# Kernel optimization log

Hardware: AMD Instinct MI355X
Metric: run time of the kernel (lower is better)

## Reference

```python
import jax, jax.numpy as jnp
import numpy as np


def setup_inputs() -> dict:
    key = jax.random.key(0)
    ks = jax.random.split(key, 6)
    B, S, H, I, E, V = 8, 512, 512, 2048, 16, 32000
    std = 0.02
    return {
        "hidden_states": jax.random.normal(ks[0], (B, S, H), dtype=jnp.float32),
        "expert_probs": jax.random.uniform(ks[1], (B, E), dtype=jnp.float32),
        "Wg": jax.random.normal(ks[2], (E, I, H), dtype=jnp.float32) * std,
        "Wu": jax.random.normal(ks[3], (E, I, H), dtype=jnp.float32) * std,
        "Wd": jax.random.normal(ks[4], (E, H, I), dtype=jnp.float32) * (std * 0.5),
        "Wout": jax.random.normal(ks[5], (V, H), dtype=jnp.float32) * std,
        "top_k": 2,
    }


def reference(hidden_states, expert_probs, Wg, Wu, Wd, Wout, top_k):
    # Per-sample top-k routing (routing is over the batch dim, not tokens).
    topk_probs, topk_ids = jax.lax.top_k(expert_probs, top_k)  # (B, k)
    topk_probs = topk_probs / (jnp.sum(topk_probs, axis=-1, keepdims=True) + 1e-8)

    B, S, H = hidden_states.shape
    combined = jnp.zeros((B, S, H), dtype=hidden_states.dtype)
    for k in range(top_k):  # top_k is a small static int (2)
        eid = topk_ids[:, k]                     # (B,)
        wg = Wg[eid]                             # (B, I, H) gathered expert weights
        wu = Wu[eid]                             # (B, I, H)
        wd = Wd[eid]                             # (B, H, I)
        gate = jax.nn.silu(jnp.einsum('bsh,bih->bsi', hidden_states, wg))
        up = jnp.einsum('bsh,bih->bsi', hidden_states, wu)
        out = jnp.einsum('bsi,bhi->bsh', gate * up, wd)
        combined = combined + topk_probs[:, k][:, None, None] * out

    # Shared output projection -> logits (B, S, V)
    return jnp.einsum('bsh,vh->bsv', combined, Wout)
```

## Files before the change

kernel.cpp:

```cpp
#include <hip/hip_runtime.h>
#include <hip/hip_bf16.h>
#include <cstdint>

typedef __attribute__((ext_vector_type(8))) short bf16x8;
typedef __attribute__((ext_vector_type(4))) float f32x4;

#define MFMA16(a, b, c) __builtin_amdgcn_mfma_f32_16x16x32_bf16((a), (b), (c), 0, 0, 0)

__device__ __forceinline__ ushort f2bf(float x) {
  union { float f; uint32_t u; } c; c.f = x;
  uint32_t r = (c.u + 0x7FFFu + ((c.u >> 16) & 1u)) >> 16;
  return (ushort)r;
}

__device__ __forceinline__ void gload_lds16(const ushort* g, ushort* l) {
  __builtin_amdgcn_global_load_lds((__attribute__((address_space(1))) void*)g,
                                   (__attribute__((address_space(3))) void*)l, 16, 0, 0);
}

template <int NW, int INSTR>
__device__ __forceinline__ void stageT(const ushort* __restrict__ tileBase, int ld,
                                       ushort* lds, int wid, int lane) {
#pragma unroll
  for (int q = 0; q < INSTR; q++) {
    int r = (wid * INSTR + q) * 8 + (lane >> 3);
    int cb = ((lane & 7) * 16) ^ ((r & 7) << 4);
    gload_lds16(tileBase + (long)r * ld + (cb >> 1), lds + (wid * INSTR + q) * 512);
  }
}

__device__ __forceinline__ bf16x8 frag_read(const ushort* lds, int r, int kb) {
  int off = r * 128 + (kb ^ ((r & 7) << 4));
  return *(const bf16x8*)((const char*)lds + off);
}

template <int INSTR>
__device__ __forceinline__ void stage32(const ushort* __restrict__ tileBase, int ld,
                                        ushort* lds, int wid, int lane) {
#pragma unroll
  for (int q = 0; q < INSTR; q++) {
    int r = (wid * INSTR + q) * 16 + (lane >> 2);
    int cb = ((lane & 3) ^ ((r >> 1) & 3)) * 16;
    gload_lds16(tileBase + (long)r * ld + (cb >> 1), lds + (wid * INSTR + q) * 512);
  }
}

__device__ __forceinline__ bf16x8 frag_read32(const ushort* lds, int r, int kslot) {
  int off = r * 64 + ((kslot ^ ((r >> 1) & 3)) * 16);
  return *(const bf16x8*)((const char*)lds + off);
}

__device__ __forceinline__ void top2(const float* __restrict__ p, int& i0, int& i1,
                                     float& p0, float& p1) {
  float v0 = -1e30f, v1 = -1e30f; i0 = 0; i1 = 0;
#pragma unroll
  for (int e = 0; e < 16; e++) {
    float v = p[e];
    if (v > v0) { v1 = v0; i1 = i0; v0 = v; i0 = e; }
    else if (v > v1) { v1 = v; i1 = e; }
  }
  float s = 1.0f / (v0 + v1 + 1e-8f);
  p0 = v0 * s; p1 = v1 * s;
}

__global__ void cvt_all(const float* __restrict__ hidden, const float* __restrict__ wout,
                        const float* __restrict__ eprobs,
                        const float* __restrict__ Wg, const float* __restrict__ Wu,
                        const float* __restrict__ Wd,
                        ushort* __restrict__ h_bf, ushort* __restrict__ wo_bf,
                        ushort* __restrict__ wg_bf, ushort* __restrict__ wu_bf,
                        ushort* __restrict__ wd_bf) {
  __shared__ unsigned smask;
  if (threadIdx.x == 0) {
    unsigned m = 0;
    for (int b = 0; b < 8; b++) {
      int i0, i1; float q0, q1;
      top2(eprobs + b * 16, i0, i1, q0, q1);
      m |= (1u << i0) | (1u << i1);
    }
    smask = m;
  }
  __syncthreads();
  const unsigned selm = smask;

  const long h4 = 2097152L / 4, w4 = 16384000L / 4;
  const long e4 = 1048576L / 4;
  const long n4 = h4 + w4 + 48 * e4;
  long stride = (long)gridDim.x * blockDim.x;
  for (long g = (long)blockIdx.x * blockDim.x + threadIdx.x; g < n4; g += stride) {
    const float* src; ushort* dst; long o;
    if (g < h4) { src = hidden; dst = h_bf; o = g; }
    else if (g < h4 + w4) { src = wout; dst = wo_bf; o = g - h4; }
    else {
      long idx = g - h4 - w4;
      int m = (int)(idx / (16 * e4));
      long rem = idx - (long)m * 16 * e4;
      int e = (int)(rem / e4);
      if (!((selm >> e) & 1u)) continue;
      src = (m == 0 ? Wg : (m == 1 ? Wu : Wd));
      dst = (m == 0 ? wg_bf : (m == 1 ? wu_bf : wd_bf));
      o = rem;
    }
    float4 v = ((const float4*)src)[o];
    ((ushort4*)dst)[o] = make_ushort4(f2bf(v.x), f2bf(v.y), f2bf(v.z), f2bf(v.w));
  }
}

__global__ __launch_bounds__(256, 4) void gateup128(
    const ushort* __restrict__ Hb, const ushort* __restrict__ Wg,
    const ushort* __restrict__ Wu, const float* __restrict__ eprobs,
    ushort* __restrict__ G) {
  constexpr int Hd = 512, I = 2048, S = 512, NTT = 16;
  __shared__ ushort As[2][128 * 32], B1s[2][64 * 32], B2s[2][64 * 32];

  int wg = blockIdx.x;
  int swz = (wg & 7) * 256 + (wg >> 3);
  int p = swz >> 7;
  int r7 = swz & 127;
  int rowT = r7 & 3, colT = r7 >> 2;
  const int b = p >> 1;
  int i0, i1; float q0, q1;
  top2(eprobs + b * 16, i0, i1, q0, q1);
  const int eid = (p & 1) ? i1 : i0;
  const int row0 = rowT * 128, col0 = colT * 64;
  const ushort* Ab  = Hb + ((long)b * S + row0) * Hd;
  const ushort* B1b = Wg + ((long)eid * I + col0) * Hd;
  const ushort* B2b = Wu + ((long)eid * I + col0) * Hd;

  const int tid = threadIdx.x, wid = tid >> 6, lane = tid & 63;
  const int wr = wid >> 1, wc = wid & 1;
  const int l15 = lane & 15;
  const int kslot = lane >> 4;

  f32x4 acc1[4][2] = {};
  f32x4 acc2[4][2] = {};

  auto stageGU = [&](int t, int buf) {
    stage32<2>(Ab + t * 32, Hd, As[buf], wid, lane);
    stage32<1>(B1b + t * 32, Hd, B1s[buf], wid, lane);
    stage32<1>(B2b + t * 32, Hd, B2s[buf], wid, lane);
  };

  stageGU(0, 0);

  for (int t = 0; t < NTT; t++) {
    if (t + 1 < NTT) {
      stageGU(t + 1, (t + 1) & 1);
      asm volatile("s_waitcnt vmcnt(4)" ::: "memory");
    } else {
      asm volatile("s_waitcnt vmcnt(0)" ::: "memory");
    }
    __builtin_amdgcn_s_barrier();
    __builtin_amdgcn_sched_barrier(0);
    const ushort* as = As[t & 1];
    bf16x8 av[4], bv[2];
#pragma unroll
    for (int i = 0; i < 4; i++) av[i] = frag_read32(as, wr * 64 + i * 16 + l15, kslot);
#pragma unroll
    for (int j = 0; j < 2; j++) bv[j] = frag_read32(B1s[t & 1], wc * 32 + j * 16 + l15, kslot);
    __builtin_amdgcn_s_setprio(1);
#pragma unroll
    for (int i = 0; i < 4; i++)
#pragma unroll
      for (int j = 0; j < 2; j++) acc1[i][j] = MFMA16(av[i], bv[j], acc1[i][j]);
    __builtin_amdgcn_s_setprio(0);
#pragma unroll
    for (int j = 0; j < 2; j++) bv[j] = frag_read32(B2s[t & 1], wc * 32 + j * 16 + l15, kslot);
    __builtin_amdgcn_s_setprio(1);
#pragma unroll
    for (int i = 0; i < 4; i++)
#pragma unroll
      for (int j = 0; j < 2; j++) acc2[i][j] = MFMA16(av[i], bv[j], acc2[i][j]);
    __builtin_amdgcn_s_setprio(0);
    asm volatile("s_waitcnt lgkmcnt(0)" ::: "memory");
    __builtin_amdgcn_sched_barrier(0);
    __builtin_amdgcn_s_barrier();
  }

  ushort* Gout = G + (long)p * S * I;
#pragma unroll
  for (int i = 0; i < 4; i++) {
    int r = row0 + wr * 64 + i * 16 + ((lane >> 4) * 4);
#pragma unroll
    for (int j = 0; j < 2; j++) {
      int c = col0 + wc * 32 + j * 16 + l15;
#pragma unroll
      for (int q = 0; q < 4; q++) {
        float g = acc1[i][j][q], u = acc2[i][j][q];
        float sg = g / (1.0f + __expf(-g));
        Gout[(long)(r + q) * I + c] = f2bf(sg * u);
      }
    }
  }
}

__global__ __launch_bounds__(256) void down_fused(
    const ushort* __restrict__ G, const ushort* __restrict__ Wd,
    const float* __restrict__ eprobs, ushort* __restrict__ Cb) {
  constexpr int I = 2048, Hd = 512, S = 512, NT = 64;
  const int b = blockIdx.z;
  const int row0 = blockIdx.x * 128, col0 = blockIdx.y * 32;
  __shared__ ushort As[2][128 * 64], Bs[2][32 * 64];
  const int tid = threadIdx.x, wid = tid >> 6, lane = tid & 63;
  int e0, e1; float p0, p1;
  top2(eprobs + b * 16, e0, e1, p0, p1);
  const ushort* A0 = G + ((long)(2 * b) * S + row0) * I;
  const ushort* A1 = G + ((long)(2 * b + 1) * S + row0) * I;
  const ushort* B0 = Wd + ((long)e0 * Hd + col0) * I;
  const ushort* B1 = Wd + ((long)e1 * Hd + col0) * I;

  f32x4 acc[2][2] = {};

  auto stageD = [&](int t2, int buf) {
    const ushort* An = (t2 < 32 ? A0 + t2 * 64 : A1 + (t2 - 32) * 64);
    const ushort* Bn = (t2 < 32 ? B0 + t2 * 64 : B1 + (t2 - 32) * 64);
    stageT<4, 4>(An, I, As[buf], wid, lane);
    stageT<4, 1>(Bn, I, Bs[buf], wid, lane);
  };

  stageD(0, 0);

  for (int t = 0; t < NT; t++) {
    if (t + 1 < NT) stageD(t + 1, (t + 1) & 1);
    if (t + 1 < NT) asm volatile("s_waitcnt vmcnt(5)" ::: "memory");
    else            asm volatile("s_waitcnt vmcnt(0)" ::: "memory");
    __builtin_amdgcn_s_barrier();
    __builtin_amdgcn_sched_barrier(0);
    if (t == 32) {
      float ratio = p0 / p1;
#pragma unroll
      for (int i = 0; i < 2; i++)
#pragma unroll
        for (int j = 0; j < 2; j++) acc[i][j] *= ratio;
    }
#pragma unroll
    for (int ks = 0; ks < 2; ks++) {
      const int kb = ks * 64 + ((lane >> 4) * 16);
      bf16x8 av[2], bv[2];
#pragma unroll
      for (int i = 0; i < 2; i++) av[i] = frag_read(As[t & 1], wid * 32 + i * 16 + (lane & 15), kb);
#pragma unroll
      for (int j = 0; j < 2; j++) bv[j] = frag_read(Bs[t & 1], j * 16 + (lane & 15), kb);
      __builtin_amdgcn_s_setprio(1);
#pragma unroll
      for (int i = 0; i < 2; i++)
#pragma unroll
        for (int j = 0; j < 2; j++) acc[i][j] = MFMA16(av[i], bv[j], acc[i][j]);
      __builtin_amdgcn_s_setprio(0);
    }
    asm volatile("s_waitcnt lgkmcnt(0)" ::: "memory");
    __builtin_amdgcn_sched_barrier(0);
    __builtin_amdgcn_s_barrier();
  }

  ushort* Co = Cb + ((long)b * S + row0) * Hd + col0;
#pragma unroll
  for (int i = 0; i < 2; i++) {
    int r = wid * 32 + i * 16 + ((lane >> 4) * 4);
#pragma unroll
    for (int j = 0; j < 2; j++) {
      int c = j * 16 + (lane & 15);
#pragma unroll
      for (int q = 0; q < 4; q++)
        Co[(long)(r + q) * Hd + c] = f2bf(p1 * acc[i][j][q]);
    }
  }
}

__global__ __launch_bounds__(256, 4) void gemm128_final(
    const ushort* __restrict__ A,
    const ushort* __restrict__ B,
    float* __restrict__ Out) {
  constexpr int K = 512, NTT = 16, LDC = 32000;
  __shared__ ushort As[2][128 * 32], Bs[2][128 * 32];

  int wg = blockIdx.x;
  int swz = (wg & 7) * 1000 + (wg >> 3);
  const int colT = swz / 32, rowT = swz % 32;
  const int row0 = rowT * 128, col0 = colT * 128;

  const int tid = threadIdx.x, wid = tid >> 6, lane = tid & 63;
  const int wr = wid >> 1, wc = wid & 1;
  const int l15 = lane & 15;
  const int kslot = lane >> 4;

  const ushort* Ab = A + (long)row0 * K;
  const ushort* Bb = B + (long)col0 * K;
  f32x4 acc[4][4] = {};

  stage32<2>(Ab, K, As[0], wid, lane);
  stage32<2>(Bb, K, Bs[0], wid, lane);

  for (int t = 0; t < NTT; t++) {
    if (t + 1 < NTT) {
      stage32<2>(Ab + (t + 1) * 32, K, As[(t + 1) & 1], wid, lane);
      stage32<2>(Bb + (t + 1) * 32, K, Bs[(t + 1) & 1], wid, lane);
      asm volatile("s_waitcnt vmcnt(4)" ::: "memory");
    } else {
      asm volatile("s_waitcnt vmcnt(0)" ::: "memory");
    }
    __builtin_amdgcn_s_barrier();
    __builtin_amdgcn_sched_barrier(0);
    const ushort* as = As[t & 1];
    const ushort* bs = Bs[t & 1];
    bf16x8 av[4], bv[4];
#pragma unroll
    for (int i = 0; i < 4; i++) av[i] = frag_read32(as, wr * 64 + i * 16 + l15, kslot);
#pragma unroll
    for (int j = 0; j < 4; j++) bv[j] = frag_read32(bs, wc * 64 + j * 16 + l15, kslot);
    __builtin_amdgcn_s_setprio(1);
#pragma unroll
    for (int i = 0; i < 4; i++)
#pragma unroll
      for (int j = 0; j < 4; j++)
        acc[i][j] = MFMA16(av[i], bv[j], acc[i][j]);
    __builtin_amdgcn_s_setprio(0);
    asm volatile("s_waitcnt lgkmcnt(0)" ::: "memory");
    __builtin_amdgcn_sched_barrier(0);
    __builtin_amdgcn_s_barrier();
  }

#pragma unroll
  for (int i = 0; i < 4; i++) {
    int r = row0 + wr * 64 + i * 16 + ((lane >> 4) * 4);
#pragma unroll
    for (int j = 0; j < 4; j++) {
      int c = col0 + wc * 64 + j * 16 + l15;
#pragma unroll
      for (int q = 0; q < 4; q++)
        __builtin_nontemporal_store(acc[i][j][q], &Out[(long)(r + q) * LDC + c]);
    }
  }
}

extern "C" void kernel_launch(void* const* d_in, const int* in_sizes, int n_in,
                              void* d_out, int out_size, void* d_ws, size_t ws_size,
                              hipStream_t stream) {
  const float* hidden = (const float*)d_in[0];
  const float* eprobs = (const float*)d_in[1];
  const float* Wg     = (const float*)d_in[2];
  const float* Wu     = (const float*)d_in[3];
  const float* Wd     = (const float*)d_in[4];
  const float* Wout   = (const float*)d_in[5];
  float* out = (float*)d_out;

  char* ws = (char*)d_ws;
  ushort* h_bf  = (ushort*)(ws + 256);
  ushort* wg_bf = h_bf  + 2097152L;
  ushort* wu_bf = wg_bf + 16777216L;
  ushort* wd_bf = wu_bf + 16777216L;
  ushort* wo_bf = wd_bf + 16777216L;
  ushort* Gbuf  = wo_bf + 16384000L;
  ushort* Cb    = Gbuf  + 16777216L;

  hipLaunchKernelGGL(cvt_all, dim3(4096), dim3(256), 0, stream,
                     hidden, Wout, eprobs, Wg, Wu, Wd, h_bf, wo_bf, wg_bf, wu_bf, wd_bf);
  hipLaunchKernelGGL(gateup128, dim3(2048), dim3(256), 0, stream,
                     h_bf, wg_bf, wu_bf, eprobs, Gbuf);
  hipLaunchKernelGGL(down_fused, dim3(4, 16, 8), dim3(256), 0, stream,
                     Gbuf, wd_bf, eprobs, Cb);
  hipLaunchKernelGGL(gemm128_final, dim3(8000), dim3(256), 0, stream, Cb, wo_bf, out);
}
```

Measured before the change: 387.2 us.

## Fuse expert weight bf16 conversion into gate-up and down GEMM loaders

Removes the separate conversion pass over the selected expert weights (Wg, Wu, Wd). The GEMM kernels now load fp32 weights into registers, pack them to bf16, and write them to LDS themselves, prefetching one tile ahead, so each weight is read once in fp32 with no bf16 round trip through global memory. In exchange the B tiles lose the direct global-to-LDS path, register pressure rises (launch bounds drop to 3 waves), and the gate-up kernel converts each expert tile once per row tile rather than once overall, which adds redundant fp32 reads and conversions.

After: 328.4 us, median of 3. 1.18x faster.

```diff
diff --git a/kernel.cpp b/kernel.cpp
--- a/kernel.cpp
+++ b/kernel.cpp
@@ -50,6 +50,15 @@
   return *(const bf16x8*)((const char*)lds + off);
 }
 
+__device__ __forceinline__ bf16x8 pack8(float4 a, float4 b) {
+  bf16x8 v;
+  v[0] = (short)f2bf(a.x); v[1] = (short)f2bf(a.y);
+  v[2] = (short)f2bf(a.z); v[3] = (short)f2bf(a.w);
+  v[4] = (short)f2bf(b.x); v[5] = (short)f2bf(b.y);
+  v[6] = (short)f2bf(b.z); v[7] = (short)f2bf(b.w);
+  return v;
+}
+
 __device__ __forceinline__ void top2(const float* __restrict__ p, int& i0, int& i1,
                                      float& p0, float& p1) {
   float v0 = -1e30f, v1 = -1e30f; i0 = 0; i1 = 0;
@@ -63,52 +72,22 @@
   p0 = v0 * s; p1 = v1 * s;
 }
 
-__global__ void cvt_all(const float* __restrict__ hidden, const float* __restrict__ wout,
-                        const float* __restrict__ eprobs,
-                        const float* __restrict__ Wg, const float* __restrict__ Wu,
-                        const float* __restrict__ Wd,
-                        ushort* __restrict__ h_bf, ushort* __restrict__ wo_bf,
-                        ushort* __restrict__ wg_bf, ushort* __restrict__ wu_bf,
-                        ushort* __restrict__ wd_bf) {
-  __shared__ unsigned smask;
-  if (threadIdx.x == 0) {
-    unsigned m = 0;
-    for (int b = 0; b < 8; b++) {
-      int i0, i1; float q0, q1;
-      top2(eprobs + b * 16, i0, i1, q0, q1);
-      m |= (1u << i0) | (1u << i1);
-    }
-    smask = m;
-  }
-  __syncthreads();
-  const unsigned selm = smask;
-
-  const long h4 = 2097152L / 4, w4 = 16384000L / 4;
-  const long e4 = 1048576L / 4;
-  const long n4 = h4 + w4 + 48 * e4;
+__global__ void cvt_hw(const float* __restrict__ hidden, const float* __restrict__ wout,
+                       ushort* __restrict__ h_bf, ushort* __restrict__ wo_bf) {
+  const long h4 = 2097152L / 4, w4 = 16384000L / 4, n4 = h4 + w4;
   long stride = (long)gridDim.x * blockDim.x;
   for (long g = (long)blockIdx.x * blockDim.x + threadIdx.x; g < n4; g += stride) {
     const float* src; ushort* dst; long o;
     if (g < h4) { src = hidden; dst = h_bf; o = g; }
-    else if (g < h4 + w4) { src = wout; dst = wo_bf; o = g - h4; }
-    else {
-      long idx = g - h4 - w4;
-      int m = (int)(idx / (16 * e4));
-      long rem = idx - (long)m * 16 * e4;
-      int e = (int)(rem / e4);
-      if (!((selm >> e) & 1u)) continue;
-      src = (m == 0 ? Wg : (m == 1 ? Wu : Wd));
-      dst = (m == 0 ? wg_bf : (m == 1 ? wu_bf : wd_bf));
-      o = rem;
-    }
+    else { src = wout; dst = wo_bf; o = g - h4; }
     float4 v = ((const float4*)src)[o];
     ((ushort4*)dst)[o] = make_ushort4(f2bf(v.x), f2bf(v.y), f2bf(v.z), f2bf(v.w));
   }
 }
 
-__global__ __launch_bounds__(256, 4) void gateup128(
-    const ushort* __restrict__ Hb, const ushort* __restrict__ Wg,
-    const ushort* __restrict__ Wu, const float* __restrict__ eprobs,
+__global__ __launch_bounds__(256, 3) void gateup128(
+    const ushort* __restrict__ Hb, const float* __restrict__ Wgf,
+    const float* __restrict__ Wuf, const float* __restrict__ eprobs,
     ushort* __restrict__ G) {
   constexpr int Hd = 512, I = 2048, S = 512, NTT = 16;
   __shared__ ushort As[2][128 * 32], B1s[2][64 * 32], B2s[2][64 * 32];
@@ -124,29 +103,43 @@
   const int eid = (p & 1) ? i1 : i0;
   const int row0 = rowT * 128, col0 = colT * 64;
   const ushort* Ab  = Hb + ((long)b * S + row0) * Hd;
-  const ushort* B1b = Wg + ((long)eid * I + col0) * Hd;
-  const ushort* B2b = Wu + ((long)eid * I + col0) * Hd;
+  const float*  B1f = Wgf + ((long)eid * I + col0) * Hd;
+  const float*  B2f = Wuf + ((long)eid * I + col0) * Hd;
 
   const int tid = threadIdx.x, wid = tid >> 6, lane = tid & 63;
   const int wr = wid >> 1, wc = wid & 1;
   const int l15 = lane & 15;
   const int kslot = lane >> 4;
+  const int rB = tid >> 2, sB = tid & 3;
 
   f32x4 acc1[4][2] = {};
   f32x4 acc2[4][2] = {};
-
-  auto stageGU = [&](int t, int buf) {
-    stage32<2>(Ab + t * 32, Hd, As[buf], wid, lane);
-    stage32<1>(B1b + t * 32, Hd, B1s[buf], wid, lane);
-    stage32<1>(B2b + t * 32, Hd, B2s[buf], wid, lane);
-  };
-
-  stageGU(0, 0);
+  float4 b1a, b1b, b2a, b2b;
+
+  auto ldB = [&](int t) {
+    const float* p1 = B1f + (long)rB * Hd + t * 32 + sB * 8;
+    const float* p2 = B2f + (long)rB * Hd + t * 32 + sB * 8;
+    b1a = *(const float4*)p1; b1b = *(const float4*)(p1 + 4);
+    b2a = *(const float4*)p2; b2b = *(const float4*)(p2 + 4);
+  };
+  auto wrB = [&](int buf) {
+    int off = rB * 64 + ((sB ^ ((rB >> 1) & 3)) * 16);
+    *(bf16x8*)((char*)B1s[buf] + off) = pack8(b1a, b1b);
+    *(bf16x8*)((char*)B2s[buf] + off) = pack8(b2a, b2b);
+  };
+
+  ldB(0);
+  stage32<2>(Ab, Hd, As[0], wid, lane);
+  asm volatile("s_waitcnt vmcnt(2)" ::: "memory");
+  wrB(0);
+  ldB(1);
+  asm volatile("s_waitcnt lgkmcnt(0)" ::: "memory");
+  __builtin_amdgcn_sched_barrier(0);
 
   for (int t = 0; t < NTT; t++) {
     if (t + 1 < NTT) {
-      stageGU(t + 1, (t + 1) & 1);
-      asm volatile("s_waitcnt vmcnt(4)" ::: "memory");
+      stage32<2>(Ab + (t + 1) * 32, Hd, As[(t + 1) & 1], wid, lane);
+      asm volatile("s_waitcnt vmcnt(10)" ::: "memory");
     } else {
       asm volatile("s_waitcnt vmcnt(0)" ::: "memory");
     }
@@ -172,6 +165,11 @@
 #pragma unroll
       for (int j = 0; j < 2; j++) acc2[i][j] = MFMA16(av[i], bv[j], acc2[i][j]);
     __builtin_amdgcn_s_setprio(0);
+    if (t + 1 < NTT) {
+      asm volatile("s_waitcnt vmcnt(2)" ::: "memory");
+      wrB((t + 1) & 1);
+      if (t + 2 < NTT) ldB(t + 2);
+    }
     asm volatile("s_waitcnt lgkmcnt(0)" ::: "memory");
     __builtin_amdgcn_sched_barrier(0);
     __builtin_amdgcn_s_barrier();
@@ -195,7 +193,7 @@
 }
 
 __global__ __launch_bounds__(256) void down_fused(
-    const ushort* __restrict__ G, const ushort* __restrict__ Wd,
+    const ushort* __restrict__ G, const float* __restrict__ Wdf,
     const float* __restrict__ eprobs, ushort* __restrict__ Cb) {
   constexpr int I = 2048, Hd = 512, S = 512, NT = 64;
   const int b = blockIdx.z;
@@ -206,24 +204,40 @@
   top2(eprobs + b * 16, e0, e1, p0, p1);
   const ushort* A0 = G + ((long)(2 * b) * S + row0) * I;
   const ushort* A1 = G + ((long)(2 * b + 1) * S + row0) * I;
-  const ushort* B0 = Wd + ((long)e0 * Hd + col0) * I;
-  const ushort* B1 = Wd + ((long)e1 * Hd + col0) * I;
+  const int rB = tid >> 3, sB = tid & 7;
 
   f32x4 acc[2][2] = {};
-
-  auto stageD = [&](int t2, int buf) {
+  float4 bda, bdb;
+
+  auto stA = [&](int t2, int buf) {
     const ushort* An = (t2 < 32 ? A0 + t2 * 64 : A1 + (t2 - 32) * 64);
-    const ushort* Bn = (t2 < 32 ? B0 + t2 * 64 : B1 + (t2 - 32) * 64);
     stageT<4, 4>(An, I, As[buf], wid, lane);
-    stageT<4, 1>(Bn, I, Bs[buf], wid, lane);
-  };
-
-  stageD(0, 0);
+  };
+  auto ldB = [&](int t2) {
+    int e = (t2 < 32) ? e0 : e1;
+    const float* pb = Wdf + ((long)e * Hd + col0 + rB) * I + (t2 & 31) * 64 + sB * 8;
+    bda = *(const float4*)pb; bdb = *(const float4*)(pb + 4);
+  };
+  auto wrB = [&](int buf) {
+    int off = rB * 128 + ((sB * 16) ^ ((rB & 7) << 4));
+    *(bf16x8*)((char*)Bs[buf] + off) = pack8(bda, bdb);
+  };
+
+  ldB(0);
+  stA(0, 0);
+  asm volatile("s_waitcnt vmcnt(4)" ::: "memory");
+  wrB(0);
+  ldB(1);
+  asm volatile("s_waitcnt lgkmcnt(0)" ::: "memory");
+  __builtin_amdgcn_sched_barrier(0);
 
   for (int t = 0; t < NT; t++) {
-    if (t + 1 < NT) stageD(t + 1, (t + 1) & 1);
-    if (t + 1 < NT) asm volatile("s_waitcnt vmcnt(5)" ::: "memory");
-    else            asm volatile("s_waitcnt vmcnt(0)" ::: "memory");
+    if (t + 1 < NT) {
+      stA(t + 1, (t + 1) & 1);
+      asm volatile("s_waitcnt vmcnt(6)" ::: "memory");
+    } else {
+      asm volatile("s_waitcnt vmcnt(0)" ::: "memory");
+    }
     __builtin_amdgcn_s_barrier();
     __builtin_amdgcn_sched_barrier(0);
     if (t == 32) {
@@ -247,6 +261,11 @@
 #pragma unroll
         for (int j = 0; j < 2; j++) acc[i][j] = MFMA16(av[i], bv[j], acc[i][j]);
       __builtin_amdgcn_s_setprio(0);
+    }
+    if (t + 1 < NT) {
+      asm volatile("s_waitcnt vmcnt(4)" ::: "memory");
+      wrB((t + 1) & 1);
+      if (t + 2 < NT) ldB(t + 2);
     }
     asm volatile("s_waitcnt lgkmcnt(0)" ::: "memory");
     __builtin_amdgcn_sched_barrier(0);
@@ -346,18 +365,14 @@
 
   char* ws = (char*)d_ws;
   ushort* h_bf  = (ushort*)(ws + 256);
-  ushort* wg_bf = h_bf  + 2097152L;
-  ushort* wu_bf = wg_bf + 16777216L;
-  ushort* wd_bf = wu_bf + 16777216L;
-  ushort* wo_bf = wd_bf + 16777216L;
+  ushort* wo_bf = h_bf  + 2097152L;
   ushort* Gbuf  = wo_bf + 16384000L;
   ushort* Cb    = Gbuf  + 16777216L;
 
-  hipLaunchKernelGGL(cvt_all, dim3(4096), dim3(256), 0, stream,
-                     hidden, Wout, eprobs, Wg, Wu, Wd, h_bf, wo_bf, wg_bf, wu_bf, wd_bf);
+  hipLaunchKernelGGL(cvt_hw, dim3(2048), dim3(256), 0, stream, hidden, Wout, h_bf, wo_bf);
   hipLaunchKernelGGL(gateup128, dim3(2048), dim3(256), 0, stream,
-                     h_bf, wg_bf, wu_bf, eprobs, Gbuf);
+                     h_bf, Wg, Wu, eprobs, Gbuf);
   hipLaunchKernelGGL(down_fused, dim3(4, 16, 8), dim3(256), 0, stream,
-                     Gbuf, wd_bf, eprobs, Cb);
+                     Gbuf, Wd, eprobs, Cb);
   hipLaunchKernelGGL(gemm128_final, dim3(8000), dim3(256), 0, stream, Cb, wo_bf, out);
 }
```
